# Optimization experiments

Hardware: AMD Instinct MI355X
Metric: run time of the kernel (lower is better)

## Reference

```python
import jax, jax.numpy as jnp
import numpy as np

N_CRY = 8192      # crystals in batch
ELEMS = 8         # sites per crystal
N = N_CRY * ELEMS # 65536 element sites
M = N_CRY * ELEMS * ELEMS  # 524288 intra-crystal pairs
AUG = 4
N_AUG = N_CRY // AUG
ELEM_EMB, SYM_EMB = 200, 444
ELEM_FEA, SYM_FEA = 32, 32
FEA = ELEM_FEA + SYM_FEA  # 64
HID = 256
N_GRAPH = 3


def _simple_net(x, W1, b1, W2, b2):
    # SimpleNetwork: Linear -> LeakyReLU -> Linear
    return jax.nn.leaky_relu(x @ W1 + b1) @ W2 + b2


def _wt_attn_pool(x, index, weights, pow_, gW1, gb1, gW2, gb2, mW1, mb1, mW2, mb2, nseg):
    # WeightedAttentionPooling: softmax-like gate scaled by weights**pow, scatter-add of messages
    gate = _simple_net(x, gW1, gb1, gW2, gb2)                      # [E,1]
    gmax = jax.ops.segment_max(gate, index, num_segments=nseg)      # [S,1]
    gate = jnp.power(weights, pow_) * jnp.exp(gate - gmax[index])
    denom = jax.ops.segment_sum(gate, index, num_segments=nseg)
    gate = gate / (denom[index] + 1e-10)
    msg = _simple_net(x, mW1, mb1, mW2, mb2)                        # [E,FEA]
    return jax.ops.segment_sum(gate * msg, index, num_segments=nseg)


def setup_inputs() -> dict:
    key = jax.random.key(0)
    ks = jax.random.split(key, 32)

    # fractional stoichiometry weights, bounded away from 0
    elem_weights = jax.random.uniform(ks[0], (N, 1), jnp.float32) * 0.9 + 0.1
    elem_fea = jax.random.normal(ks[1], (N, ELEM_EMB), jnp.float32)
    sym_fea = jax.random.normal(ks[2], (N, SYM_EMB), jnp.float32)

    # structured graph: fully-connected pairs within each crystal of ELEMS sites
    base = np.arange(N_CRY, dtype=np.int32)[:, None, None] * ELEMS
    self_idx = jnp.asarray((base + np.arange(ELEMS, dtype=np.int32)[:, None]).repeat(ELEMS, axis=2).reshape(-1))
    nbr_idx = jnp.asarray(np.broadcast_to(base + np.arange(ELEMS, dtype=np.int32)[None, None, :], (N_CRY, ELEMS, ELEMS)).reshape(-1).copy())
    cry_elem_idx = jnp.asarray(np.arange(N, dtype=np.int32) // ELEMS)
    aug_cry_idx = jnp.asarray(np.arange(N_CRY, dtype=np.int32) // AUG)

    def lin(k, fi, fo):
        s = 1.0 / np.sqrt(fi)
        kw, kb = jax.random.split(k)
        return (jax.random.uniform(kw, (fi, fo), jnp.float32, -s, s),
                jax.random.uniform(kb, (fo,), jnp.float32, -s, s))

    elem_W, elem_b = lin(ks[3], ELEM_EMB, ELEM_FEA)
    sym_W, sym_b = lin(ks[4], SYM_EMB + 1, SYM_FEA)

    def stack_lin(k, fi, fo, n):
        Ws, bs = [], []
        for kk in jax.random.split(k, n):
            W, b = lin(kk, fi, fo)
            Ws.append(W); bs.append(b)
        return jnp.stack(Ws), jnp.stack(bs)

    g_gate_W1, g_gate_b1 = stack_lin(ks[5], 2 * FEA, HID, N_GRAPH)
    g_gate_W2, g_gate_b2 = stack_lin(ks[6], HID, 1, N_GRAPH)
    g_msg_W1, g_msg_b1 = stack_lin(ks[7], 2 * FEA, HID, N_GRAPH)
    g_msg_W2, g_msg_b2 = stack_lin(ks[8], HID, FEA, N_GRAPH)
    g_pow = jax.random.normal(ks[9], (N_GRAPH,), jnp.float32) * 0.5

    c_gate_W1, c_gate_b1 = lin(ks[10], FEA, HID)
    c_gate_W2, c_gate_b2 = lin(ks[11], HID, 1)
    c_msg_W1, c_msg_b1 = lin(ks[12], FEA, HID)
    c_msg_W2, c_msg_b2 = lin(ks[13], HID, FEA)
    c_pow = jax.random.normal(ks[14], (), jnp.float32) * 0.5

    return dict(elem_weights=elem_weights, elem_fea=elem_fea, sym_fea=sym_fea,
                self_idx=self_idx, nbr_idx=nbr_idx, cry_elem_idx=cry_elem_idx,
                aug_cry_idx=aug_cry_idx,
                elem_W=elem_W, elem_b=elem_b, sym_W=sym_W, sym_b=sym_b,
                g_gate_W1=g_gate_W1, g_gate_b1=g_gate_b1, g_gate_W2=g_gate_W2, g_gate_b2=g_gate_b2,
                g_msg_W1=g_msg_W1, g_msg_b1=g_msg_b1, g_msg_W2=g_msg_W2, g_msg_b2=g_msg_b2,
                g_pow=g_pow,
                c_gate_W1=c_gate_W1, c_gate_b1=c_gate_b1, c_gate_W2=c_gate_W2, c_gate_b2=c_gate_b2,
                c_msg_W1=c_msg_W1, c_msg_b1=c_msg_b1, c_msg_W2=c_msg_W2, c_msg_b2=c_msg_b2,
                c_pow=c_pow)


def reference(elem_weights, elem_fea, sym_fea, self_idx, nbr_idx, cry_elem_idx, aug_cry_idx,
              elem_W, elem_b, sym_W, sym_b,
              g_gate_W1, g_gate_b1, g_gate_W2, g_gate_b2,
              g_msg_W1, g_msg_b1, g_msg_W2, g_msg_b2, g_pow,
              c_gate_W1, c_gate_b1, c_gate_W2, c_gate_b2,
              c_msg_W1, c_msg_b1, c_msg_W2, c_msg_b2, c_pow):
    # embed element and Wyckoff features
    e = elem_fea @ elem_W + elem_b                                   # [N,32]
    s = jnp.concatenate([sym_fea, elem_weights], axis=1) @ sym_W + sym_b  # [N,32]
    fea = jnp.concatenate([e, s], axis=1)                            # [N,64]

    nbr_w = elem_weights[nbr_idx]                                    # [M,1]
    for l in range(N_GRAPH):
        pair = jnp.concatenate([fea[self_idx], fea[nbr_idx]], axis=1)  # [M,128]
        msg = _wt_attn_pool(pair, self_idx, nbr_w, g_pow[l],
                            g_gate_W1[l], g_gate_b1[l], g_gate_W2[l], g_gate_b2[l],
                            g_msg_W1[l], g_msg_b1[l], g_msg_W2[l], g_msg_b2[l], N)
        fea = fea + msg  # single elem head -> mean over heads is identity; residual

    # crystal pooling (single head -> mean is identity)
    head = _wt_attn_pool(fea, cry_elem_idx, elem_weights, c_pow,
                         c_gate_W1, c_gate_b1, c_gate_W2, c_gate_b2,
                         c_msg_W1, c_msg_b1, c_msg_W2, c_msg_b2, N_CRY)  # [N_CRY,64]

    # scatter_mean over augmentation groups
    sums = jax.ops.segment_sum(head, aug_cry_idx, num_segments=N_AUG)
    cnts = jax.ops.segment_sum(jnp.ones((N_CRY,), head.dtype), aug_cry_idx, num_segments=N_AUG)
    return sums / cnts[:, None]                                      # [N_AUG,64]
```

## Files before the change

### kernel.cpp

```cpp
#include <hip/hip_runtime.h>
#include <math.h>

#define NBLK 1024

typedef _Float16 f16x2 __attribute__((ext_vector_type(2)));
typedef _Float16 f16x8 __attribute__((ext_vector_type(8)));
typedef __fp16   h16x2 __attribute__((ext_vector_type(2)));
typedef __fp16   h16x8 __attribute__((ext_vector_type(8)));
typedef float    f32x4 __attribute__((ext_vector_type(4)));

struct Params {
  const float* elem_weights; const float* elem_fea; const float* sym_fea;
  const float* elem_W; const float* elem_b; const float* sym_W; const float* sym_b;
  const float* g_gate_W1; const float* g_gate_b1; const float* g_gate_W2; const float* g_gate_b2;
  const float* g_msg_W1;  const float* g_msg_b1;  const float* g_msg_W2;  const float* g_msg_b2;
  const float* g_pow;
  const float* c_gate_W1; const float* c_gate_b1; const float* c_gate_W2; const float* c_gate_b2;
  const float* c_msg_W1;  const float* c_msg_b1;  const float* c_msg_W2;  const float* c_msg_b2;
  const float* c_pow;
  float* out;
};

#define SZ_EW   7168
#define SZ_SW   14336
#define SZ_GW1  32768
#define SZ_MW2  16384
#define SZ_CW1  16384
#define SZ_CW2  16384
#define OFF_EW   0
#define OFF_SW   (OFF_EW + SZ_EW)
#define OFF_GW1  (OFF_SW + SZ_SW)
#define OFF_MW1  (OFF_GW1 + 3*SZ_GW1)
#define OFF_MW2  (OFF_MW1 + 3*SZ_GW1)
#define OFF_CGW1 (OFF_MW2 + 3*SZ_MW2)
#define OFF_CMW1 (OFF_CGW1 + SZ_CW1)
#define OFF_CMW2 (OFF_CMW1 + SZ_CW1)
#define OFF_W2P  (OFF_CMW2 + SZ_CW2)
#define OFF_CW2P (OFF_W2P + 768)
#define WS_TOTAL (OFF_CW2P + 256)

__device__ __forceinline__ unsigned h2u(f16x2 h) { return __builtin_bit_cast(unsigned, h); }
__device__ __forceinline__ f16x2 u2h(unsigned u) { return __builtin_bit_cast(f16x2, u); }
__device__ __forceinline__ unsigned pkrtz(float a, float b) {
  return __builtin_bit_cast(unsigned, __builtin_amdgcn_cvt_pkrtz(a, b));
}
__device__ __forceinline__ f16x2 lrelu2(f16x2 x) {
  const f16x2 c01 = {(_Float16)0.01f, (_Float16)0.01f};
  return __builtin_elementwise_max(x, x * c01);
}
#if __has_builtin(__builtin_amdgcn_fdot2)
__device__ __forceinline__ float dot2f(f16x2 a, f16x2 b, float c) {
  return __builtin_amdgcn_fdot2(__builtin_bit_cast(h16x2, a),
                                __builtin_bit_cast(h16x2, b), c, false);
}
#else
__device__ __forceinline__ float dot2f(f16x2 a, f16x2 b, float c) {
  return c + (float)a[0] * (float)b[0] + (float)a[1] * (float)b[1];
}
#endif
__device__ __forceinline__ f16x8 cvt8h(float4 x, float4 y) {
  uint4 u;
  u.x = pkrtz(x.x, x.y); u.y = pkrtz(x.z, x.w);
  u.z = pkrtz(y.x, y.y); u.w = pkrtz(y.z, y.w);
  return __builtin_bit_cast(f16x8, u);
}
__device__ __forceinline__ f32x4 mfma16(f16x8 a, f16x8 b, f32x4 c) {
  return __builtin_amdgcn_mfma_f32_16x16x32_f16(__builtin_bit_cast(h16x8, a),
                                                __builtin_bit_cast(h16x8, b), c, 0, 0, 0);
}
__device__ __forceinline__ int permL(int l) { return l ^ ((l >> 4) & 3); }

__global__ void __launch_bounds__(256) pack_frags(Params p, unsigned short* ws) {
  const int idx = blockIdx.x * 256 + threadIdx.x;
  if (idx >= WS_TOTAL) return;
  float v = 0.f;
  if (idx < OFF_SW) {
    const int q = idx, mt = q / 3584, r = q % 3584, ks = r >> 9, w = r & 511;
    const int l = w >> 3, e = w & 7;
    const int m = mt * 16 + (l & 15), k = ks * 32 + ((l >> 4) << 3) + e;
    v = (k < 200) ? p.elem_W[k * 32 + m] : 0.f;
  } else if (idx < OFF_GW1) {
    const int q = idx - OFF_SW, mt = q / 7168, r = q % 7168, ks = r >> 9, w = r & 511;
    const int l = w >> 3, e = w & 7;
    const int m = mt * 16 + (l & 15), k = ks * 32 + ((l >> 4) << 3) + e;
    v = (k < 445) ? p.sym_W[k * 32 + m] : 0.f;
  } else if (idx < OFF_MW1) {
    const int q = idx - OFF_GW1, layer = q >> 15, r = q & 32767;
    const int mt = r >> 10, r2 = r & 1023, ks = r2 >> 9, w = r2 & 511;
    const int l = w >> 3, e = w & 7;
    const int m = mt * 16 + (l & 15), k = ks * 32 + ((l >> 4) << 3) + e;
    v = p.g_gate_W1[(size_t)layer * 32768 + (k + (m >> 8) * 64) * 256 + (m & 255)];
  } else if (idx < OFF_MW2) {
    const int q = idx - OFF_MW1, layer = q >> 15, r = q & 32767;
    const int mt = r >> 10, r2 = r & 1023, ks = r2 >> 9, w = r2 & 511;
    const int l = w >> 3, e = w & 7;
    const int m = mt * 16 + (l & 15), k = ks * 32 + ((l >> 4) << 3) + e;
    v = p.g_msg_W1[(size_t)layer * 32768 + (k + (m >> 8) * 64) * 256 + (m & 255)];
  } else if (idx < OFF_CGW1) {
    const int q = idx - OFF_MW2, layer = q / 16384, r = q % 16384;
    const int mt = r >> 12, r2 = r & 4095, ks = r2 >> 9, w = r2 & 511;
    const int l = w >> 3, e = w & 7;
    const int m = mt * 16 + (l & 15), k = ks * 32 + ((l >> 4) << 3) + e;
    v = p.g_msg_W2[(size_t)layer * 16384 + k * 64 + m];
  } else if (idx < OFF_CMW1) {
    const int q = idx - OFF_CGW1, mt = q >> 10, r2 = q & 1023, ks = r2 >> 9, w = r2 & 511;
    const int l = w >> 3, e = w & 7;
    const int m = mt * 16 + (l & 15), k = ks * 32 + ((l >> 4) << 3) + e;
    v = p.c_gate_W1[k * 256 + m];
  } else if (idx < OFF_CMW2) {
    const int q = idx - OFF_CMW1, mt = q >> 10, r2 = q & 1023, ks = r2 >> 9, w = r2 & 511;
    const int l = w >> 3, e = w & 7;
    const int m = mt * 16 + (l & 15), k = ks * 32 + ((l >> 4) << 3) + e;
    v = p.c_msg_W1[k * 256 + m];
  } else if (idx < OFF_W2P) {
    const int q = idx - OFF_CMW2, mt = q >> 12, r2 = q & 4095, ks = r2 >> 9, w = r2 & 511;
    const int l = w >> 3, e = w & 7;
    const int m = mt * 16 + (l & 15), k = ks * 32 + ((l >> 4) << 3) + e;
    v = p.c_msg_W2[k * 64 + m];
  } else if (idx < OFF_CW2P) {
    v = p.g_gate_W2[idx - OFF_W2P];
  } else {
    v = p.c_gate_W2[idx - OFF_CW2P];
  }
  const _Float16 h = (_Float16)v;
  ws[idx] = __builtin_bit_cast(unsigned short, h);
}

template<int MT>
__device__ __forceinline__ void w1g2(const unsigned short* frag, const unsigned short* feaBf,
                                     int X, unsigned short* U, unsigned short* V,
                                     const float* biasU, const float* biasV,
                                     int mtBase, int col, int g, int lane) {
  f16x8 bf[2][2];
  #pragma unroll
  for (int nt2 = 0; nt2 < 2; ++nt2)
    #pragma unroll
    for (int ks = 0; ks < 2; ++ks)
      bf[nt2][ks] = *(const f16x8*)&feaBf[((ks * 4 + X * 2 + nt2) << 9) + (lane << 3)];
  const unsigned short* fp = frag + ((mtBase * 2) << 9) + (lane << 3);
  f16x8 a0 = *(const f16x8*)(fp);
  f16x8 a1 = *(const f16x8*)(fp + 512);
  #pragma unroll
  for (int i = 0; i < MT; ++i) {
    f16x8 n0, n1;
    if (i + 1 < MT) {
      n0 = *(const f16x8*)(fp + (i + 1) * 1024);
      n1 = *(const f16x8*)(fp + (i + 1) * 1024 + 512);
    }
    f32x4 acc0 = {0.f, 0.f, 0.f, 0.f}, acc1 = {0.f, 0.f, 0.f, 0.f};
    acc0 = mfma16(a0, bf[0][0], acc0); acc0 = mfma16(a1, bf[0][1], acc0);
    acc1 = mfma16(a0, bf[1][0], acc1); acc1 = mfma16(a1, bf[1][1], acc1);
    const int m0 = (mtBase + i) * 16 + g * 4;
    unsigned short* base;
    int mo;
    float4 bv = {0.f, 0.f, 0.f, 0.f};
    if (m0 < 256) {
      base = U; mo = m0;
      if (biasU) bv = *(const float4*)&biasU[m0];
    } else {
      base = V; mo = m0 - 256;
      if (biasV) bv = *(const float4*)&biasV[m0 - 256];
    }
    acc0[0] += bv.x; acc0[1] += bv.y; acc0[2] += bv.z; acc0[3] += bv.w;
    acc1[0] += bv.x; acc1[1] += bv.y; acc1[2] += bv.z; acc1[3] += bv.w;
    *(uint2*)&base[col * 264 + mo]        = (uint2){pkrtz(acc0[0], acc0[1]), pkrtz(acc0[2], acc0[3])};
    *(uint2*)&base[(16 + col) * 264 + mo] = (uint2){pkrtz(acc1[0], acc1[1]), pkrtz(acc1[2], acc1[3])};
    if (i + 1 < MT) { a0 = n0; a1 = n1; }
  }
}

template<int MT>
__device__ __forceinline__ void cw1g4(const unsigned short* frag, const unsigned short* feaBf,
                                      unsigned short* Uc, const float* bias,
                                      int mtBase, int col, int g, int lane) {
  f16x8 cf[4][2];
  #pragma unroll
  for (int nt = 0; nt < 4; ++nt)
    #pragma unroll
    for (int ks = 0; ks < 2; ++ks)
      cf[nt][ks] = *(const f16x8*)&feaBf[((ks * 4 + nt) << 9) + (lane << 3)];
  const unsigned short* fp = frag + ((mtBase * 2) << 9) + (lane << 3);
  f16x8 a0 = *(const f16x8*)(fp);
  f16x8 a1 = *(const f16x8*)(fp + 512);
  #pragma unroll
  for (int i = 0; i < MT; ++i) {
    f16x8 n0, n1;
    if (i + 1 < MT) {
      n0 = *(const f16x8*)(fp + (i + 1) * 1024);
      n1 = *(const f16x8*)(fp + (i + 1) * 1024 + 512);
    }
    const int m0 = (mtBase + i) * 16 + g * 4;
    const float4 bv = *(const float4*)&bias[m0];
    #pragma unroll
    for (int nt = 0; nt < 4; ++nt) {
      f32x4 acc = {0.f, 0.f, 0.f, 0.f};
      acc = mfma16(a0, cf[nt][0], acc); acc = mfma16(a1, cf[nt][1], acc);
      acc[0] += bv.x; acc[1] += bv.y; acc[2] += bv.z; acc[3] += bv.w;
      *(uint2*)&Uc[(nt * 16 + col) * 264 + m0] = (uint2){pkrtz(acc[0], acc[1]), pkrtz(acc[2], acc[3])};
    }
    if (i + 1 < MT) { a0 = n0; a1 = n1; }
  }
}

__device__ __forceinline__ void phaseB(const unsigned short* U, const unsigned short* V,
                                       const unsigned short* w2p, float gb2, float gpow,
                                       const float* ewL, float* gsumAll, unsigned* gateH,
                                       int X, int t) {
  const int crl = t >> 6, s = (t >> 3) & 7, j = t & 7;
  const unsigned short* Urow = U + (crl * 8 + s) * 264;
  const unsigned short* Vrow = V + (crl * 8 + j) * 264;
  const uint4* w2g = (const uint4*)w2p;
  float lg0 = 0.f, lg1 = 0.f, lg2 = 0.f, lg3 = 0.f;
  #pragma unroll 8
  for (int i = 0; i < 32; ++i) {
    const uint4 uu = *(const uint4*)&Urow[i * 8];
    const uint4 vv = *(const uint4*)&Vrow[i * 8];
    const uint4 wv = w2g[i];
    lg0 = dot2f(lrelu2(u2h(uu.x) + u2h(vv.x)), u2h(wv.x), lg0);
    lg1 = dot2f(lrelu2(u2h(uu.y) + u2h(vv.y)), u2h(wv.y), lg1);
    lg2 = dot2f(lrelu2(u2h(uu.z) + u2h(vv.z)), u2h(wv.z), lg2);
    lg3 = dot2f(lrelu2(u2h(uu.w) + u2h(vv.w)), u2h(wv.w), lg3);
  }
  float lg = ((lg0 + lg1) + (lg2 + lg3)) + gb2;
  float mx = lg;
  mx = fmaxf(mx, __shfl_xor(mx, 1));
  mx = fmaxf(mx, __shfl_xor(mx, 2));
  mx = fmaxf(mx, __shfl_xor(mx, 4));
  const float ewn = ewL[X * 32 + crl * 8 + j];
  float e = __expf(gpow * __logf(ewn)) * __expf(lg - mx);
  float sm = e;
  sm += __shfl_xor(sm, 1);
  sm += __shfl_xor(sm, 2);
  sm += __shfl_xor(sm, 4);
  const float gt = e / (sm + 1e-10f);
  gateH[X * 256 + t] = pkrtz(gt, gt);
  if (j == 0) gsumAll[X * 32 + crl * 8 + s] = sm / (sm + 1e-10f);
}

__device__ __forceinline__ void phaseC(unsigned short* U, const unsigned short* V,
                                       const unsigned* gateH, int X, int t) {
  const int hp = t & 127, ch = (t >> 7) & 1;
  #pragma unroll
  for (int cc = 0; cc < 2; ++cc) {
    const int crl = ch * 2 + cc;
    unsigned vmb[8];
    #pragma unroll
    for (int j = 0; j < 8; ++j) vmb[j] = *(const unsigned*)&V[(crl * 8 + j) * 264 + 2 * hp];
    #pragma unroll
    for (int s = 0; s < 8; ++s) {
      const f16x2 um2 = u2h(*(const unsigned*)&U[(crl * 8 + s) * 264 + 2 * hp]);
      const uint4 g0 = *(const uint4*)&gateH[X * 256 + crl * 64 + s * 8];
      const uint4 g1 = *(const uint4*)&gateH[X * 256 + crl * 64 + s * 8 + 4];
      f16x2 accA = {(_Float16)0.f, (_Float16)0.f};
      f16x2 accB = {(_Float16)0.f, (_Float16)0.f};
      accA += lrelu2(um2 + u2h(vmb[0])) * u2h(g0.x);
      accA += lrelu2(um2 + u2h(vmb[1])) * u2h(g0.y);
      accA += lrelu2(um2 + u2h(vmb[2])) * u2h(g0.z);
      accA += lrelu2(um2 + u2h(vmb[3])) * u2h(g0.w);
      accB += lrelu2(um2 + u2h(vmb[4])) * u2h(g1.x);
      accB += lrelu2(um2 + u2h(vmb[5])) * u2h(g1.y);
      accB += lrelu2(um2 + u2h(vmb[6])) * u2h(g1.z);
      accB += lrelu2(um2 + u2h(vmb[7])) * u2h(g1.w);
      *(unsigned*)&U[(crl * 8 + s) * 264 + 2 * hp] = h2u(accA + accB);
    }
  }
}

__global__ void __launch_bounds__(512)
__attribute__((amdgpu_waves_per_eu(4, 4)))
wren_fused(Params p, const unsigned short* ws) {
  const int t    = threadIdx.x;
  const int blk  = blockIdx.x;
  const int wid  = t >> 6;
  const int lane = t & 63;
  const int col  = lane & 15, g = lane >> 4;

  __shared__ __align__(16) unsigned short lds[37888];
  unsigned short* feaBf = lds;
  unsigned short* UgA = lds + 4096;
  unsigned short* VgA = lds + 12544;
  unsigned short* UgB = lds + 20992;
  unsigned short* VgB = lds + 29440;
  float* S = (float*)(lds + 4096);
  unsigned short* stg = lds + 12800;
  __shared__ __align__(16) unsigned gateH[512];
  __shared__ __align__(16) float ewL[64];
  __shared__ __align__(16) float gsumAll[64];
  __shared__ __align__(16) unsigned gcH[64];
  __shared__ __align__(16) float cLog[64];
  __shared__ __align__(16) float gscAll[8];

  if (t < 64) ewL[t] = p.elem_weights[blk * 64 + t];
  __syncthreads();

  const int mtE = wid >> 2, ntE = wid & 3;
  const int sSite = t >> 3, sTk = t & 7;
  const int sNt = sSite >> 4, sS15 = sSite & 15;

  {
    const size_t gbase = (size_t)(blk * 64 + sSite) * 200;
    #pragma unroll
    for (int it = 0; it < 4; ++it) {
      const int c = sTk + it * 8;
      if (c < 28) {
        const int idx = (((c >> 2) * 4 + sNt) << 9) + (permL((c & 3) * 16 + sS15) << 3);
        if (c < 25) {
          const float4 v0 = *(const float4*)(p.elem_fea + gbase + c * 8);
          const float4 v1 = *(const float4*)(p.elem_fea + gbase + c * 8 + 4);
          *(uint4*)&stg[idx] = __builtin_bit_cast(uint4, cvt8h(v0, v1));
        } else {
          *(uint4*)&stg[idx] = (uint4){0u, 0u, 0u, 0u};
        }
      }
    }
  }
  __syncthreads();
  {
    f32x4 acc = {0.f, 0.f, 0.f, 0.f};
    const unsigned short* ap = ws + OFF_EW + ((mtE * 7) << 9) + (lane << 3);
    f16x8 aw = *(const f16x8*)ap;
    #pragma unroll
    for (int ks = 0; ks < 7; ++ks) {
      f16x8 nx;
      if (ks < 6) nx = *(const f16x8*)(ap + (ks + 1) * 512);
      const f16x8 bin = *(const f16x8*)&stg[((ks * 4 + ntE) << 9) + (permL(lane) << 3)];
      acc = mfma16(aw, bin, acc);
      if (ks < 6) aw = nx;
    }
    const int site = ntE * 16 + col;
    const int f0 = mtE * 16 + g * 4;
    const float4 bv = *(const float4*)&p.elem_b[f0];
    float4 o = {acc[0] + bv.x, acc[1] + bv.y, acc[2] + bv.z, acc[3] + bv.w};
    *(float4*)&S[site * 68 + f0] = o;
    const int lt = ((mtE * 2 + (g >> 1)) << 4) | col;
    const int e0 = (g & 1) * 4;
    *(uint2*)&feaBf[((0 * 4 + ntE) << 9) + lt * 8 + e0] = (uint2){pkrtz(o.x, o.y), pkrtz(o.z, o.w)};
  }
  __syncthreads();
  {
    f32x4 accS = {0.f, 0.f, 0.f, 0.f};
    const size_t gbase = (size_t)(blk * 64 + sSite) * 444;
    const float ewv = ewL[sSite];
    #pragma unroll
    for (int h = 0; h < 2; ++h) {
      #pragma unroll
      for (int it = 0; it < 4; ++it) {
        const int c = h * 28 + sTk + it * 8;
        if (c < (h + 1) * 28) {
          const int ksl = (c >> 2) - h * 7;
          const int idx = ((ksl * 4 + sNt) << 9) + (permL((c & 3) * 16 + sS15) << 3);
          if (c < 55) {
            const float4 v0 = *(const float4*)(p.sym_fea + gbase + c * 8);
            const float4 v1 = *(const float4*)(p.sym_fea + gbase + c * 8 + 4);
            *(uint4*)&stg[idx] = __builtin_bit_cast(uint4, cvt8h(v0, v1));
          } else {
            const float4 v0 = *(const float4*)(p.sym_fea + gbase + 440);
            f16x8 bin;
            bin[0] = (_Float16)v0.x; bin[1] = (_Float16)v0.y;
            bin[2] = (_Float16)v0.z; bin[3] = (_Float16)v0.w;
            bin[4] = (_Float16)ewv;
            bin[5] = (_Float16)0.f; bin[6] = (_Float16)0.f; bin[7] = (_Float16)0.f;
            *(uint4*)&stg[idx] = __builtin_bit_cast(uint4, bin);
          }
        }
      }
      __syncthreads();
      {
        const unsigned short* ap = ws + OFF_SW + ((mtE * 14 + h * 7) << 9) + (lane << 3);
        f16x8 aw = *(const f16x8*)ap;
        #pragma unroll
        for (int ks = 0; ks < 7; ++ks) {
          f16x8 nx;
          if (ks < 6) nx = *(const f16x8*)(ap + (ks + 1) * 512);
          const f16x8 bin = *(const f16x8*)&stg[((ks * 4 + ntE) << 9) + (permL(lane) << 3)];
          accS = mfma16(aw, bin, accS);
          if (ks < 6) aw = nx;
        }
      }
      __syncthreads();
    }
    const int site = ntE * 16 + col;
    const int f0 = mtE * 16 + g * 4;
    const float4 bv = *(const float4*)&p.sym_b[f0];
    float4 o = {accS[0] + bv.x, accS[1] + bv.y, accS[2] + bv.z, accS[3] + bv.w};
    *(float4*)&S[site * 68 + 32 + f0] = o;
    const int lt = ((mtE * 2 + (g >> 1)) << 4) | col;
    const int e0 = (g & 1) * 4;
    *(uint2*)&feaBf[((1 * 4 + ntE) << 9) + lt * 8 + e0] = (uint2){pkrtz(o.x, o.y), pkrtz(o.z, o.w)};
  }
  __syncthreads();

  const int myX  = (wid >= 4) ? 0 : 1;
  const int myFw = (wid >= 4) ? wid - 4 : wid;
  float4 regM0, regM1;
  {
    const int f0 = myFw * 16 + g * 4;
    regM0 = *(const float4*)&S[(myX * 32 + col) * 68 + f0];
    regM1 = *(const float4*)&S[(myX * 32 + 16 + col) * 68 + f0];
  }
  __syncthreads();

  w1g2<4>(ws + OFF_GW1, feaBf, 0, UgA, VgA, p.g_gate_b1, nullptr, wid * 4, col, g, lane);
  __syncthreads();

  for (int l = 0; l < 3; ++l) {
    const unsigned short* fragG  = ws + OFF_GW1 + l * SZ_GW1;
    const unsigned short* fragM  = ws + OFF_MW1 + l * SZ_GW1;
    const unsigned short* fragW2 = ws + OFF_MW2 + l * SZ_MW2;
    const unsigned short* w2p    = ws + OFF_W2P + l * 256;
    const float gb2  = p.g_gate_b2[l];
    const float gpow = p.g_pow[l];
    const float* gB1 = p.g_gate_b1 + l * 256;
    const float* mB1 = p.g_msg_b1 + l * 256;

    if (wid < 4) phaseB(UgA, VgA, w2p, gb2, gpow, ewL, gsumAll, gateH, 0, t);
    else w1g2<8>(fragG, feaBf, 1, UgB, VgB, gB1, nullptr, (wid - 4) * 8, col, g, lane);
    __syncthreads();

    if (wid < 4) phaseB(UgB, VgB, w2p, gb2, gpow, ewL, gsumAll, gateH, 1, t);
    else w1g2<8>(fragM, feaBf, 0, UgA, VgA, nullptr, mB1, (wid - 4) * 8, col, g, lane);
    __syncthreads();

    if (wid < 4) phaseC(UgA, VgA, gateH, 0, t);
    else w1g2<8>(fragM, feaBf, 1, UgB, VgB, nullptr, mB1, (wid - 4) * 8, col, g, lane);
    __syncthreads();

    if (wid < 4) {
      phaseC(UgB, VgB, gateH, 1, t);
    } else {
      f32x4 accw[2] = {{0.f, 0.f, 0.f, 0.f}, {0.f, 0.f, 0.f, 0.f}};
      const unsigned short* wp = fragW2 + ((myFw * 8) << 9) + (lane << 3);
      f16x8 aw = *(const f16x8*)wp;
      #pragma unroll
      for (int ks = 0; ks < 8; ++ks) {
        f16x8 nx;
        if (ks < 7) nx = *(const f16x8*)(wp + (ks + 1) * 512);
        #pragma unroll
        for (int nt2 = 0; nt2 < 2; ++nt2) {
          const f16x8 bh = *(const f16x8*)&UgA[(nt2 * 16 + col) * 264 + ks * 32 + g * 8];
          accw[nt2] = mfma16(aw, bh, accw[nt2]);
        }
        if (ks < 7) aw = nx;
      }
      const int f0 = myFw * 16 + g * 4;
      const float4 mb2v = *(const float4*)&p.g_msg_b2[l * 64 + f0];
      const int ks2 = myFw >> 1, fh = myFw & 1;
      const int lt2 = ((fh * 2 + (g >> 1)) << 4) | col;
      const int e02 = (g & 1) * 4;
      {
        const float gs = gsumAll[col];
        regM0.x += accw[0][0] + gs * mb2v.x; regM0.y += accw[0][1] + gs * mb2v.y;
        regM0.z += accw[0][2] + gs * mb2v.z; regM0.w += accw[0][3] + gs * mb2v.w;
        *(uint2*)&feaBf[((ks2 * 4 + 0) << 9) + lt2 * 8 + e02] =
            (uint2){pkrtz(regM0.x, regM0.y), pkrtz(regM0.z, regM0.w)};
      }
      {
        const float gs = gsumAll[16 + col];
        regM1.x += accw[1][0] + gs * mb2v.x; regM1.y += accw[1][1] + gs * mb2v.y;
        regM1.z += accw[1][2] + gs * mb2v.z; regM1.w += accw[1][3] + gs * mb2v.w;
        *(uint2*)&feaBf[((ks2 * 4 + 1) << 9) + lt2 * 8 + e02] =
            (uint2){pkrtz(regM1.x, regM1.y), pkrtz(regM1.z, regM1.w)};
      }
    }
    __syncthreads();

    if (wid < 4) {
      f32x4 accw[2] = {{0.f, 0.f, 0.f, 0.f}, {0.f, 0.f, 0.f, 0.f}};
      const unsigned short* wp = fragW2 + ((myFw * 8) << 9) + (lane << 3);
      f16x8 aw = *(const f16x8*)wp;
      #pragma unroll
      for (int ks = 0; ks < 8; ++ks) {
        f16x8 nx;
        if (ks < 7) nx = *(const f16x8*)(wp + (ks + 1) * 512);
        #pragma unroll
        for (int nt2 = 0; nt2 < 2; ++nt2) {
          const f16x8 bh = *(const f16x8*)&UgB[(nt2 * 16 + col) * 264 + ks * 32 + g * 8];
          accw[nt2] = mfma16(aw, bh, accw[nt2]);
        }
        if (ks < 7) aw = nx;
      }
      const int f0 = myFw * 16 + g * 4;
      const float4 mb2v = *(const float4*)&p.g_msg_b2[l * 64 + f0];
      const int ks2 = myFw >> 1, fh = myFw & 1;
      const int lt2 = ((fh * 2 + (g >> 1)) << 4) | col;
      const int e02 = (g & 1) * 4;
      {
        const float gs = gsumAll[32 + col];
        regM0.x += accw[0][0] + gs * mb2v.x; regM0.y += accw[0][1] + gs * mb2v.y;
        regM0.z += accw[0][2] + gs * mb2v.z; regM0.w += accw[0][3] + gs * mb2v.w;
        *(uint2*)&feaBf[((ks2 * 4 + 2) << 9) + lt2 * 8 + e02] =
            (uint2){pkrtz(regM0.x, regM0.y), pkrtz(regM0.z, regM0.w)};
      }
      {
        const float gs = gsumAll[48 + col];
        regM1.x += accw[1][0] + gs * mb2v.x; regM1.y += accw[1][1] + gs * mb2v.y;
        regM1.z += accw[1][2] + gs * mb2v.z; regM1.w += accw[1][3] + gs * mb2v.w;
        *(uint2*)&feaBf[((ks2 * 4 + 3) << 9) + lt2 * 8 + e02] =
            (uint2){pkrtz(regM1.x, regM1.y), pkrtz(regM1.z, regM1.w)};
      }
    } else if (l < 2) {
      w1g2<8>(ws + OFF_GW1 + (l + 1) * SZ_GW1, feaBf, 0, UgA, VgA,
              p.g_gate_b1 + (l + 1) * 256, nullptr, (wid - 4) * 8, col, g, lane);
    }
    __syncthreads();
  }

  const float cpow = p.c_pow[0];
  const float cgb2 = p.c_gate_b2[0];
  unsigned short* Uc = lds + 4096;
  unsigned short* Hc = lds + 20992;

  cw1g4<2>(ws + OFF_CGW1, feaBf, Uc, p.c_gate_b1, wid * 2, col, g, lane);
  __syncthreads();

  {
    const unsigned short* Ur = &Uc[(t >> 3) * 264];
    const int hh = t & 7;
    const uint4* cw2g = (const uint4*)(ws + OFF_CW2P);
    float pa = 0.f, pb = 0.f;
    #pragma unroll
    for (int i = 0; i < 4; ++i) {
      const uint4 uu = *(const uint4*)&Ur[hh * 32 + i * 8];
      const uint4 wv = cw2g[hh * 4 + i];
      pa = dot2f(lrelu2(u2h(uu.x)), u2h(wv.x), pa);
      pa = dot2f(lrelu2(u2h(uu.y)), u2h(wv.y), pa);
      pb = dot2f(lrelu2(u2h(uu.z)), u2h(wv.z), pb);
      pb = dot2f(lrelu2(u2h(uu.w)), u2h(wv.w), pb);
    }
    float prt = pa + pb;
    prt += __shfl_xor(prt, 1);
    prt += __shfl_xor(prt, 2);
    prt += __shfl_xor(prt, 4);
    if (hh == 0) cLog[t >> 3] = prt;
  }
  __syncthreads();

  if (t < 64) {
    float gl = cLog[t] + cgb2;
    float mx = gl;
    mx = fmaxf(mx, __shfl_xor(mx, 1));
    mx = fmaxf(mx, __shfl_xor(mx, 2));
    mx = fmaxf(mx, __shfl_xor(mx, 4));
    float e = __expf(cpow * __logf(ewL[t])) * __expf(gl - mx);
    float sm = e;
    sm += __shfl_xor(sm, 1);
    sm += __shfl_xor(sm, 2);
    sm += __shfl_xor(sm, 4);
    const float gc = e / (sm + 1e-10f);
    gcH[t] = pkrtz(gc, gc);
    if ((t & 7) == 0) gscAll[t >> 3] = sm / (sm + 1e-10f);
  }
  cw1g4<2>(ws + OFF_CMW1, feaBf, Uc, p.c_msg_b1, wid * 2, col, g, lane);
  __syncthreads();

  {
    const int hp = t & 127, qq = t >> 7;
    *(unsigned*)&Hc[(8 + qq * 2) * 264 + 2 * hp] = 0u;
    *(unsigned*)&Hc[(9 + qq * 2) * 264 + 2 * hp] = 0u;
    #pragma unroll
    for (int cc = 0; cc < 2; ++cc) {
      const int ci = qq * 2 + cc;
      f16x2 acc = {(_Float16)0.f, (_Float16)0.f};
      #pragma unroll
      for (int s = 0; s < 8; ++s) {
        const f16x2 um2 = u2h(*(const unsigned*)&Uc[(ci * 8 + s) * 264 + 2 * hp]);
        acc += lrelu2(um2) * u2h(gcH[ci * 8 + s]);
      }
      *(unsigned*)&Hc[ci * 264 + 2 * hp] = h2u(acc);
    }
  }
  __syncthreads();

  if (wid < 4) {
    f32x4 accf = {0.f, 0.f, 0.f, 0.f};
    const unsigned short* wp = ws + OFF_CMW2 + ((wid * 8) << 9) + (lane << 3);
    f16x8 aw = *(const f16x8*)wp;
    #pragma unroll
    for (int ks = 0; ks < 8; ++ks) {
      f16x8 nx;
      if (ks < 7) nx = *(const f16x8*)(wp + (ks + 1) * 512);
      const f16x8 bh = *(const f16x8*)&Hc[col * 264 + ks * 32 + g * 8];
      accf = mfma16(aw, bh, accf);
      if (ks < 7) aw = nx;
    }
    float vr[4];
    #pragma unroll
    for (int reg = 0; reg < 4; ++reg) {
      float v = accf[reg];
      v += __shfl_xor(v, 1);
      v += __shfl_xor(v, 2);
      vr[reg] = v;
    }
    if (col == 0 || col == 4) {
      const int aug = 2 * blk + (col >> 2);
      const float sgc = (col == 0) ? (gscAll[0] + gscAll[1] + gscAll[2] + gscAll[3])
                                   : (gscAll[4] + gscAll[5] + gscAll[6] + gscAll[7]);
      const int f0 = wid * 16 + g * 4;
      const float4 cb = *(const float4*)&p.c_msg_b2[f0];
      float4 o = {0.25f * (vr[0] + sgc * cb.x), 0.25f * (vr[1] + sgc * cb.y),
                  0.25f * (vr[2] + sgc * cb.z), 0.25f * (vr[3] + sgc * cb.w)};
      *(float4*)&p.out[(size_t)aug * 64 + f0] = o;
    }
  }
}

extern "C" void kernel_launch(void* const* d_in, const int* in_sizes, int n_in,
                              void* d_out, int out_size, void* d_ws, size_t ws_size,
                              hipStream_t stream) {
  (void)in_sizes; (void)n_in; (void)out_size; (void)ws_size;
  Params p;
  p.elem_weights = (const float*)d_in[0];
  p.elem_fea     = (const float*)d_in[1];
  p.sym_fea      = (const float*)d_in[2];
  p.elem_W    = (const float*)d_in[7];
  p.elem_b    = (const float*)d_in[8];
  p.sym_W     = (const float*)d_in[9];
  p.sym_b     = (const float*)d_in[10];
  p.g_gate_W1 = (const float*)d_in[11];
  p.g_gate_b1 = (const float*)d_in[12];
  p.g_gate_W2 = (const float*)d_in[13];
  p.g_gate_b2 = (const float*)d_in[14];
  p.g_msg_W1  = (const float*)d_in[15];
  p.g_msg_b1  = (const float*)d_in[16];
  p.g_msg_W2  = (const float*)d_in[17];
  p.g_msg_b2  = (const float*)d_in[18];
  p.g_pow     = (const float*)d_in[19];
  p.c_gate_W1 = (const float*)d_in[20];
  p.c_gate_b1 = (const float*)d_in[21];
  p.c_gate_W2 = (const float*)d_in[22];
  p.c_gate_b2 = (const float*)d_in[23];
  p.c_msg_W1  = (const float*)d_in[24];
  p.c_msg_b1  = (const float*)d_in[25];
  p.c_msg_W2  = (const float*)d_in[26];
  p.c_msg_b2  = (const float*)d_in[27];
  p.c_pow     = (const float*)d_in[28];
  p.out       = (float*)d_out;

  unsigned short* ws = (unsigned short*)d_ws;
  hipLaunchKernelGGL(pack_frags, dim3((WS_TOTAL + 255) / 256), dim3(256), 0, stream, p, ws);
  hipLaunchKernelGGL(wren_fused, dim3(NBLK), dim3(512), 0, stream, p, ws);
}
```

Measured before the change: 144.2 us.

## Replace warp-specialized ping-pong schedule with all-wave phased execution per layer

The graph-layer loop drops the producer/consumer split, where half the waves ran the attention gate and gated reduction while the other half ran the next W1 GEMM. Now all eight waves run each phase together: gate W1 for both halves, then gate softmax over all crystals, then message W1, then gated reduce, then W2 with each wave group handling one half. This balances the work across waves and removes the extra prologue GEMM, but it gives up the overlap between MFMA and VALU phases. The number of barriers per layer stays about the same.

```diff
diff --git a/kernel.cpp b/kernel.cpp
--- a/kernel.cpp
+++ b/kernel.cpp
@@ -202,11 +202,15 @@
   }
 }
 
-__device__ __forceinline__ void phaseB(const unsigned short* U, const unsigned short* V,
-                                       const unsigned short* w2p, float gb2, float gpow,
-                                       const float* ewL, float* gsumAll, unsigned* gateH,
-                                       int X, int t) {
-  const int crl = t >> 6, s = (t >> 3) & 7, j = t & 7;
+__device__ __forceinline__ void phaseB_all(const unsigned short* UgA, const unsigned short* VgA,
+                                           const unsigned short* UgB, const unsigned short* VgB,
+                                           const unsigned short* w2p, float gb2, float gpow,
+                                           const float* ewL, float* gsumAll, unsigned* gateH,
+                                           int t) {
+  const int cr = t >> 6, s = (t >> 3) & 7, j = t & 7;
+  const unsigned short* U = (cr < 4) ? UgA : UgB;
+  const unsigned short* V = (cr < 4) ? VgA : VgB;
+  const int crl = cr & 3;
   const unsigned short* Urow = U + (crl * 8 + s) * 264;
   const unsigned short* Vrow = V + (crl * 8 + j) * 264;
   const uint4* w2g = (const uint4*)w2p;
@@ -226,43 +230,44 @@
   mx = fmaxf(mx, __shfl_xor(mx, 1));
   mx = fmaxf(mx, __shfl_xor(mx, 2));
   mx = fmaxf(mx, __shfl_xor(mx, 4));
-  const float ewn = ewL[X * 32 + crl * 8 + j];
+  const float ewn = ewL[cr * 8 + j];
   float e = __expf(gpow * __logf(ewn)) * __expf(lg - mx);
   float sm = e;
   sm += __shfl_xor(sm, 1);
   sm += __shfl_xor(sm, 2);
   sm += __shfl_xor(sm, 4);
   const float gt = e / (sm + 1e-10f);
-  gateH[X * 256 + t] = pkrtz(gt, gt);
-  if (j == 0) gsumAll[X * 32 + crl * 8 + s] = sm / (sm + 1e-10f);
-}
-
-__device__ __forceinline__ void phaseC(unsigned short* U, const unsigned short* V,
-                                       const unsigned* gateH, int X, int t) {
-  const int hp = t & 127, ch = (t >> 7) & 1;
+  gateH[t] = pkrtz(gt, gt);
+  if (j == 0) gsumAll[cr * 8 + s] = sm / (sm + 1e-10f);
+}
+
+__device__ __forceinline__ void phaseC_all(unsigned short* UgA, const unsigned short* VgA,
+                                           unsigned short* UgB, const unsigned short* VgB,
+                                           const unsigned* gateH, int t) {
+  const int cr = t >> 6, hq = t & 63;
+  unsigned short* U = (cr < 4) ? UgA : UgB;
+  const unsigned short* V = (cr < 4) ? VgA : VgB;
+  const int crl = cr & 3;
+  uint2 vmb[8];
   #pragma unroll
-  for (int cc = 0; cc < 2; ++cc) {
-    const int crl = ch * 2 + cc;
-    unsigned vmb[8];
-    #pragma unroll
-    for (int j = 0; j < 8; ++j) vmb[j] = *(const unsigned*)&V[(crl * 8 + j) * 264 + 2 * hp];
-    #pragma unroll
-    for (int s = 0; s < 8; ++s) {
-      const f16x2 um2 = u2h(*(const unsigned*)&U[(crl * 8 + s) * 264 + 2 * hp]);
-      const uint4 g0 = *(const uint4*)&gateH[X * 256 + crl * 64 + s * 8];
-      const uint4 g1 = *(const uint4*)&gateH[X * 256 + crl * 64 + s * 8 + 4];
-      f16x2 accA = {(_Float16)0.f, (_Float16)0.f};
-      f16x2 accB = {(_Float16)0.f, (_Float16)0.f};
-      accA += lrelu2(um2 + u2h(vmb[0])) * u2h(g0.x);
-      accA += lrelu2(um2 + u2h(vmb[1])) * u2h(g0.y);
-      accA += lrelu2(um2 + u2h(vmb[2])) * u2h(g0.z);
-      accA += lrelu2(um2 + u2h(vmb[3])) * u2h(g0.w);
-      accB += lrelu2(um2 + u2h(vmb[4])) * u2h(g1.x);
-      accB += lrelu2(um2 + u2h(vmb[5])) * u2h(g1.y);
-      accB += lrelu2(um2 + u2h(vmb[6])) * u2h(g1.z);
-      accB += lrelu2(um2 + u2h(vmb[7])) * u2h(g1.w);
-      *(unsigned*)&U[(crl * 8 + s) * 264 + 2 * hp] = h2u(accA + accB);
-    }
+  for (int j = 0; j < 8; ++j) vmb[j] = *(const uint2*)&V[(crl * 8 + j) * 264 + 4 * hq];
+  #pragma unroll
+  for (int s = 0; s < 8; ++s) {
+    const uint2 um2 = *(const uint2*)&U[(crl * 8 + s) * 264 + 4 * hq];
+    const f16x2 umA = u2h(um2.x), umB = u2h(um2.y);
+    const uint4 g0 = *(const uint4*)&gateH[cr * 64 + s * 8];
+    const uint4 g1 = *(const uint4*)&gateH[cr * 64 + s * 8 + 4];
+    f16x2 aA = {(_Float16)0.f, (_Float16)0.f};
+    f16x2 aB = {(_Float16)0.f, (_Float16)0.f};
+    aA += lrelu2(umA + u2h(vmb[0].x)) * u2h(g0.x);  aB += lrelu2(umB + u2h(vmb[0].y)) * u2h(g0.x);
+    aA += lrelu2(umA + u2h(vmb[1].x)) * u2h(g0.y);  aB += lrelu2(umB + u2h(vmb[1].y)) * u2h(g0.y);
+    aA += lrelu2(umA + u2h(vmb[2].x)) * u2h(g0.z);  aB += lrelu2(umB + u2h(vmb[2].y)) * u2h(g0.z);
+    aA += lrelu2(umA + u2h(vmb[3].x)) * u2h(g0.w);  aB += lrelu2(umB + u2h(vmb[3].y)) * u2h(g0.w);
+    aA += lrelu2(umA + u2h(vmb[4].x)) * u2h(g1.x);  aB += lrelu2(umB + u2h(vmb[4].y)) * u2h(g1.x);
+    aA += lrelu2(umA + u2h(vmb[5].x)) * u2h(g1.y);  aB += lrelu2(umB + u2h(vmb[5].y)) * u2h(g1.y);
+    aA += lrelu2(umA + u2h(vmb[6].x)) * u2h(g1.z);  aB += lrelu2(umB + u2h(vmb[6].y)) * u2h(g1.z);
+    aA += lrelu2(umA + u2h(vmb[7].x)) * u2h(g1.w);  aB += lrelu2(umB + u2h(vmb[7].y)) * u2h(g1.w);
+    *(uint2*)&U[(crl * 8 + s) * 264 + 4 * hq] = (uint2){h2u(aA), h2u(aB)};
   }
 }
 
@@ -400,9 +405,6 @@
   }
   __syncthreads();
 
-  w1g2<4>(ws + OFF_GW1, feaBf, 0, UgA, VgA, p.g_gate_b1, nullptr, wid * 4, col, g, lane);
-  __syncthreads();
-
   for (int l = 0; l < 3; ++l) {
     const unsigned short* fragG  = ws + OFF_GW1 + l * SZ_GW1;
     const unsigned short* fragM  = ws + OFF_MW1 + l * SZ_GW1;
@@ -413,21 +415,23 @@
     const float* gB1 = p.g_gate_b1 + l * 256;
     const float* mB1 = p.g_msg_b1 + l * 256;
 
-    if (wid < 4) phaseB(UgA, VgA, w2p, gb2, gpow, ewL, gsumAll, gateH, 0, t);
-    else w1g2<8>(fragG, feaBf, 1, UgB, VgB, gB1, nullptr, (wid - 4) * 8, col, g, lane);
+    w1g2<4>(fragG, feaBf, 0, UgA, VgA, gB1, nullptr, wid * 4, col, g, lane);
+    w1g2<4>(fragG, feaBf, 1, UgB, VgB, gB1, nullptr, wid * 4, col, g, lane);
     __syncthreads();
 
-    if (wid < 4) phaseB(UgB, VgB, w2p, gb2, gpow, ewL, gsumAll, gateH, 1, t);
-    else w1g2<8>(fragM, feaBf, 0, UgA, VgA, nullptr, mB1, (wid - 4) * 8, col, g, lane);
+    phaseB_all(UgA, VgA, UgB, VgB, w2p, gb2, gpow, ewL, gsumAll, gateH, t);
     __syncthreads();
 
-    if (wid < 4) phaseC(UgA, VgA, gateH, 0, t);
-    else w1g2<8>(fragM, feaBf, 1, UgB, VgB, nullptr, mB1, (wid - 4) * 8, col, g, lane);
+    w1g2<4>(fragM, feaBf, 0, UgA, VgA, nullptr, mB1, wid * 4, col, g, lane);
+    w1g2<4>(fragM, feaBf, 1, UgB, VgB, nullptr, mB1, wid * 4, col, g, lane);
     __syncthreads();
 
-    if (wid < 4) {
-      phaseC(UgB, VgB, gateH, 1, t);
-    } else {
+    phaseC_all(UgA, VgA, UgB, VgB, gateH, t);
+    __syncthreads();
+
+    {
+      const unsigned short* Hb = (wid >= 4) ? UgA : UgB;
+      const int gsBase = myX * 32;
       f32x4 accw[2] = {{0.f, 0.f, 0.f, 0.f}, {0.f, 0.f, 0.f, 0.f}};
       const unsigned short* wp = fragW2 + ((myFw * 8) << 9) + (lane << 3);
       f16x8 aw = *(const f16x8*)wp;
@@ -437,7 +441,7 @@
         if (ks < 7) nx = *(const f16x8*)(wp + (ks + 1) * 512);
         #pragma unroll
         for (int nt2 = 0; nt2 < 2; ++nt2) {
-          const f16x8 bh = *(const f16x8*)&UgA[(nt2 * 16 + col) * 264 + ks * 32 + g * 8];
+          const f16x8 bh = *(const f16x8*)&Hb[(nt2 * 16 + col) * 264 + ks * 32 + g * 8];
           accw[nt2] = mfma16(aw, bh, accw[nt2]);
         }
         if (ks < 7) aw = nx;
@@ -448,59 +452,19 @@
       const int lt2 = ((fh * 2 + (g >> 1)) << 4) | col;
       const int e02 = (g & 1) * 4;
       {
-        const float gs = gsumAll[col];
+        const float gs = gsumAll[gsBase + col];
         regM0.x += accw[0][0] + gs * mb2v.x; regM0.y += accw[0][1] + gs * mb2v.y;
         regM0.z += accw[0][2] + gs * mb2v.z; regM0.w += accw[0][3] + gs * mb2v.w;
-        *(uint2*)&feaBf[((ks2 * 4 + 0) << 9) + lt2 * 8 + e02] =
+        *(uint2*)&feaBf[((ks2 * 4 + myX * 2 + 0) << 9) + lt2 * 8 + e02] =
             (uint2){pkrtz(regM0.x, regM0.y), pkrtz(regM0.z, regM0.w)};
       }
       {
-        const float gs = gsumAll[16 + col];
+        const float gs = gsumAll[gsBase + 16 + col];
         regM1.x += accw[1][0] + gs * mb2v.x; regM1.y += accw[1][1] + gs * mb2v.y;
         regM1.z += accw[1][2] + gs * mb2v.z; regM1.w += accw[1][3] + gs * mb2v.w;
-        *(uint2*)&feaBf[((ks2 * 4 + 1) << 9) + lt2 * 8 + e02] =
+        *(uint2*)&feaBf[((ks2 * 4 + myX * 2 + 1) << 9) + lt2 * 8 + e02] =
             (uint2){pkrtz(regM1.x, regM1.y), pkrtz(regM1.z, regM1.w)};
       }
-    }
-    __syncthreads();
-
-    if (wid < 4) {
-      f32x4 accw[2] = {{0.f, 0.f, 0.f, 0.f}, {0.f, 0.f, 0.f, 0.f}};
-      const unsigned short* wp = fragW2 + ((myFw * 8) << 9) + (lane << 3);
-      f16x8 aw = *(const f16x8*)wp;
-      #pragma unroll
-      for (int ks = 0; ks < 8; ++ks) {
-        f16x8 nx;
-        if (ks < 7) nx = *(const f16x8*)(wp + (ks + 1) * 512);
-        #pragma unroll
-        for (int nt2 = 0; nt2 < 2; ++nt2) {
-          const f16x8 bh = *(const f16x8*)&UgB[(nt2 * 16 + col) * 264 + ks * 32 + g * 8];
-          accw[nt2] = mfma16(aw, bh, accw[nt2]);
-        }
-        if (ks < 7) aw = nx;
-      }
-      const int f0 = myFw * 16 + g * 4;
-      const float4 mb2v = *(const float4*)&p.g_msg_b2[l * 64 + f0];
-      const int ks2 = myFw >> 1, fh = myFw & 1;
-      const int lt2 = ((fh * 2 + (g >> 1)) << 4) | col;
-      const int e02 = (g & 1) * 4;
-      {
-        const float gs = gsumAll[32 + col];
-        regM0.x += accw[0][0] + gs * mb2v.x; regM0.y += accw[0][1] + gs * mb2v.y;
-        regM0.z += accw[0][2] + gs * mb2v.z; regM0.w += accw[0][3] + gs * mb2v.w;
-        *(uint2*)&feaBf[((ks2 * 4 + 2) << 9) + lt2 * 8 + e02] =
-            (uint2){pkrtz(regM0.x, regM0.y), pkrtz(regM0.z, regM0.w)};
-      }
-      {
-        const float gs = gsumAll[48 + col];
-        regM1.x += accw[1][0] + gs * mb2v.x; regM1.y += accw[1][1] + gs * mb2v.y;
-        regM1.z += accw[1][2] + gs * mb2v.z; regM1.w += accw[1][3] + gs * mb2v.w;
-        *(uint2*)&feaBf[((ks2 * 4 + 3) << 9) + lt2 * 8 + e02] =
-            (uint2){pkrtz(regM1.x, regM1.y), pkrtz(regM1.z, regM1.w)};
-      }
-    } else if (l < 2) {
-      w1g2<8>(ws + OFF_GW1 + (l + 1) * SZ_GW1, feaBf, 0, UgA, VgA,
-              p.g_gate_b1 + (l + 1) * 256, nullptr, (wid - 4) * 8, col, g, lane);
     }
     __syncthreads();
   }
```

Result: faster. 134.6 us (-6.6%).
